# Kernel tuning notes

Hardware: AMD Instinct MI355X
Metric: run time of the kernel (lower is better)

The kernel has to match this reference:

```python
import jax, jax.numpy as jnp
import numpy as np

B, T, C, H = 2, 512, 1024, 16
D = C // H          # head dim 64
CS = 64             # chunk_size
NS_STEPS = 5
OMEGA_W = 8
KCONV = 4

# Polar Express per-iteration quintic coefficients (Amsel et al. 2025)
_PE_COEFFS = [
    (8.28721201814563, -23.595886519098837, 17.300387312530933),
    (4.107059111542203, -2.9478499167379106, 0.5448431082926601),
    (3.9486908534822946, -2.908902115962949, 0.5518191394370137),
    (3.3184196573706015, -2.488488024314874, 0.51004894012372),
    (2.300652019954817, -1.6689039845747493, 0.4188073119525673),
    (1.891301407787398, -1.2679958271945868, 0.37680408948524835),
    (1.8750014808534479, -1.2500016453999487, 0.3750001645474248),
    (1.875, -1.25, 0.375),
]

def _polar_express(X):
    # X: (..., D, D). Normalize to spectral-norm <= 1 via Frobenius bound, then iterate.
    nrm = jnp.sqrt(jnp.sum(X * X, axis=(-2, -1), keepdims=True)) + 1e-7
    Xn = X / (nrm * 1.01)
    for a, b, c in _PE_COEFFS[:NS_STEPS]:
        A = Xn @ jnp.swapaxes(Xn, -1, -2)
        Xn = a * Xn + (b * A + c * (A @ A)) @ Xn
    return Xn

def _polar_express_ste(X):
    # straight-through: forward = PE(X), backward = identity
    return X + jax.lax.stop_gradient(_polar_express(X) - X)

def _rms_norm(x):
    return x * jax.lax.rsqrt(jnp.mean(x * x, axis=-1, keepdims=True) + 1e-6)

def _poly_features(x):
    # phi(x) = sum_{i=1..p} x^i / i!  with poly_degree=2
    return x + 0.5 * x * x

def _short_conv(x, w, b):
    # causal depthwise conv; x:(B,T,C), w:(C,1,K), b:(C,)
    xc = jnp.transpose(x, (0, 2, 1))
    xc = jnp.pad(xc, ((0, 0), (0, 0), (KCONV - 1, 0)))
    y = jax.lax.conv_general_dilated(
        xc, w, window_strides=(1,), padding="VALID",
        dimension_numbers=("NCW", "OIW", "NCW"), feature_group_count=x.shape[-1])
    y = y + b[:, None]
    return jnp.transpose(y, (0, 2, 1))

def _linear_scan(h_init, gates, inputs):
    # h_t = g_t * h_{t-1} + in_t ; gates (B,cs,H), inputs (B,cs,H,D,D)
    g = gates[..., None, None]
    first = g[:, :1] * h_init[:, None] + inputs[:, :1]
    mod_in = jnp.concatenate([first, inputs[:, 1:]], axis=1)
    mod_g = jnp.concatenate([jnp.zeros_like(g[:, :1]), g[:, 1:]], axis=1)
    def comb(a, b):
        ga, xa = a; gb, xb = b
        return (ga * gb, gb * xa + xb)
    _, h_all = jax.lax.associative_scan(comb, (mod_g, mod_in), axis=1)
    return h_all, h_all[:, -1]

def _omega_aggregate(u, gamma):
    # sliding-window sum of gamma_i * u_i over last OMEGA_W positions, via cumsum
    cs = u.shape[1]
    cum = jnp.cumsum(gamma * u, axis=1)
    if OMEGA_W >= cs:
        return cum
    shifted = jnp.concatenate([jnp.zeros_like(cum[:, :OMEGA_W]), cum[:, :-OMEGA_W]], axis=1)
    return cum - shifted


def setup_inputs() -> dict:
    key = jax.random.key(0)
    ks = jax.random.split(key, 16)
    s = 0.02
    return {
        "x":   jax.random.normal(ks[0], (B, T, C), jnp.float32),
        "Wq":  jax.random.normal(ks[1], (C, C), jnp.float32) * s,
        "Wk":  jax.random.normal(ks[2], (C, C), jnp.float32) * s,
        "Wv":  jax.random.normal(ks[3], (C, C), jnp.float32) * s,
        "Wo":  jax.random.normal(ks[4], (C, C), jnp.float32) * s,
        "cqw": jax.random.normal(ks[5], (C, 1, KCONV), jnp.float32) * s,
        "cqb": jnp.zeros((C,), jnp.float32),
        "ckw": jax.random.normal(ks[6], (C, 1, KCONV), jnp.float32) * s,
        "ckb": jnp.zeros((C,), jnp.float32),
        "cvw": jax.random.normal(ks[7], (C, 1, KCONV), jnp.float32) * s,
        "cvb": jnp.zeros((C,), jnp.float32),
        "Wa":  jax.random.normal(ks[8], (H, C), jnp.float32) * s,
        "We":  jax.random.normal(ks[9], (H, C), jnp.float32) * s,
        "Wt":  jax.random.normal(ks[10], (H, C), jnp.float32) * s,
        "Wg":  jax.random.normal(ks[11], (H, C), jnp.float32) * s,
    }


def reference(x, Wq, Wk, Wv, Wo, cqw, cqb, ckw, ckb, cvw, cvb, Wa, We, Wt, Wg):
    Bsz, Tlen, Cdim = x.shape
    q = _short_conv(x @ Wq.T, cqw, cqb).reshape(Bsz, Tlen, H, D)
    k = _short_conv(x @ Wk.T, ckw, ckb).reshape(Bsz, Tlen, H, D)
    v = _short_conv(x @ Wv.T, cvw, cvb).reshape(Bsz, Tlen, H, D)
    q = _poly_features(_rms_norm(q))
    k = _poly_features(_rms_norm(k))
    alpha = jax.nn.sigmoid(x @ Wa.T)   # (B,T,H) memory retention gate
    eta   = jax.nn.sigmoid(x @ We.T)   # learning rate gate
    theta = jax.nn.sigmoid(x @ Wt.T)   # momentum gate
    gamma = jax.nn.sigmoid(x @ Wg.T)   # omega context gate

    nC = Tlen // CS
    def chunked(a):  # (B,T,...) -> (nC,B,CS,...)
        return jnp.moveaxis(a.reshape(Bsz, nC, CS, *a.shape[2:]), 1, 0)
    qc, kc, vc = chunked(q), chunked(k), chunked(v)
    ac, ec, tc, gc = chunked(alpha), chunked(eta), chunked(theta), chunked(gamma)

    M0 = jnp.zeros((Bsz, H, D, D), x.dtype)
    S0 = jnp.zeros((Bsz, H, D, D), x.dtype)

    def step(carry, inp):
        M, S = carry
        q_c, k_c, v_c, a_c, e_c, t_c, g_c = inp
        pred = jnp.einsum("bhvk,bchk->bchv", M, k_c)
        err = pred - v_c
        u = 2.0 * jnp.einsum("bchv,bchk->bchvk", err, k_c)     # per-token gradient
        u = _omega_aggregate(u, g_c[..., None, None])           # omega window
        mom_in = -(e_c[..., None, None] * u)
        chunk_S, S = _linear_scan(S, t_c, mom_in)               # momentum scan
        chunk_S_orth = _polar_express_ste(chunk_S)              # orthogonalize
        M_all, M = _linear_scan(M, a_c, chunk_S_orth)           # memory scan
        y_c = jnp.einsum("bchvk,bchk->bchv", M_all, q_c)        # read memory
        return (M, S), y_c

    _, ys = jax.lax.scan(step, (M0, S0), (qc, kc, vc, ac, ec, tc, gc))
    y = jnp.moveaxis(ys, 0, 1).reshape(Bsz, Tlen, H, D)
    y = _rms_norm(y).reshape(Bsz, Tlen, Cdim)
    return y @ Wo.T
```

## Files before the change

### kernel.cpp

```cpp
#include <hip/hip_runtime.h>

constexpr int Bsz = 2, Tsz = 512, Csz = 1024, Hsz = 16, Dsz = 64, CSz = 64;
constexpr int NCHUNK = 8, OW = 8;

typedef __attribute__((ext_vector_type(8))) _Float16 half8;
typedef __attribute__((ext_vector_type(4))) _Float16 half4;
typedef __attribute__((ext_vector_type(2))) _Float16 half2v;
typedef __attribute__((ext_vector_type(2))) __fp16 fp16x2;
typedef __attribute__((ext_vector_type(16))) float f32x16;

constexpr float INV_S = 1.0f / 2048.0f;

union H4u { half4 v; half2v p[2]; };

__device__ __forceinline__ void split_f16(float v, _Float16& hi, _Float16& lo) {
  _Float16 h = (_Float16)v;
  float r = v - (float)h;
  hi = h;
  lo = (_Float16)(r * 2048.0f);
}

__device__ __forceinline__ void split2(float a, float b, half2v& h, half2v& l) {
  fp16x2 hh = __builtin_amdgcn_cvt_pkrtz(a, b);
  half2v hv = __builtin_bit_cast(half2v, hh);
  float ra = (a - (float)hv[0]) * 2048.0f;
  float rb = (b - (float)hv[1]) * 2048.0f;
  h = hv;
  l = __builtin_bit_cast(half2v, __builtin_amdgcn_cvt_pkrtz(ra, rb));
}

#define MFMA3(accH, accL1, accL2, ah, al, bh, bl)                             \
  accH = __builtin_amdgcn_mfma_f32_32x32x16_f16(ah, bh, accH, 0, 0, 0);       \
  accL1 = __builtin_amdgcn_mfma_f32_32x32x16_f16(ah, bl, accL1, 0, 0, 0);     \
  accL2 = __builtin_amdgcn_mfma_f32_32x32x16_f16(al, bh, accL2, 0, 0, 0);

__device__ __forceinline__ void xcd_decode(int bid, int& bh, int& idx) {
  bh = (((bid >> 3) & 3) << 3) + (bid & 7);
  idx = bid >> 5;
}

__global__ __launch_bounds__(256) void split_all_kernel(
    const float* __restrict__ x, const float* __restrict__ Wq,
    const float* __restrict__ Wk, const float* __restrict__ Wv,
    const float* __restrict__ Wo, const float* __restrict__ Wa,
    const float* __restrict__ We, const float* __restrict__ Wt,
    const float* __restrict__ Wg,
    _Float16* __restrict__ xh, _Float16* __restrict__ xl,
    _Float16* __restrict__ Wqh, _Float16* __restrict__ Wql,
    _Float16* __restrict__ Wkh, _Float16* __restrict__ Wkl,
    _Float16* __restrict__ Wvh, _Float16* __restrict__ Wvl,
    _Float16* __restrict__ Woh, _Float16* __restrict__ Wol,
    _Float16* __restrict__ gWh, _Float16* __restrict__ gWl) {
  const int y = blockIdx.y;
  const int tid = threadIdx.x;
  if (y < 5) {
    const float* src = (y == 0 ? x : y == 1 ? Wq : y == 2 ? Wk : y == 3 ? Wv : Wo);
    _Float16* dh = (y == 0 ? xh : y == 1 ? Wqh : y == 2 ? Wkh : y == 3 ? Wvh : Woh);
    _Float16* dl = (y == 0 ? xl : y == 1 ? Wql : y == 2 ? Wkl : y == 3 ? Wvl : Wol);
    size_t i = ((size_t)blockIdx.x * 256 + tid) * 4;
    float4 v = *(const float4*)(src + i);
    H4u h, l;
    split2(v.x, v.y, h.p[0], l.p[0]);
    split2(v.z, v.w, h.p[1], l.p[1]);
    *(half4*)(dh + i) = h.v;
    *(half4*)(dl + i) = l.v;
  } else {
    if (blockIdx.x >= 64) return;
    size_t i = ((size_t)blockIdx.x * 256 + tid) * 4;
    int gsel = (int)(i >> 14);
    int off = (int)(i & 16383);
    const float* src = (gsel == 0 ? Wa : gsel == 1 ? We : gsel == 2 ? Wt : Wg);
    float4 v = *(const float4*)(src + off);
    H4u h, l;
    split2(v.x, v.y, h.p[0], l.p[0]);
    split2(v.z, v.w, h.p[1], l.p[1]);
    *(half4*)(gWh + i) = h.v;
    *(half4*)(gWl + i) = l.v;
  }
}

__device__ __forceinline__ void gemm64_core(const _Float16* __restrict__ Agh,
                                            const _Float16* __restrict__ Agl,
                                            const _Float16* __restrict__ Bgh,
                                            const _Float16* __restrict__ Bgl,
                                            int m0, int n0, int tid, char* LB,
                                            f32x16& accH, f32x16& accL1, f32x16& accL2) {
  const int lane = tid & 63, wv = tid >> 6;
  const int mb = (wv >> 1) << 5, nb = (wv & 1) << 5;
  const int lr = tid >> 2;
  const int lch = (tid & 3) << 4;
  const int cb = lch << 1;
  const int wb0 = (lr << 7) + (cb ^ ((lr & 7) << 4));
  const int wb1 = (lr << 7) + ((cb + 16) ^ ((lr & 7) << 4));
  const _Float16* pah = Agh + (size_t)(m0 + lr) * Csz + lch;
  const _Float16* pal = Agl + (size_t)(m0 + lr) * Csz + lch;
  const _Float16* pbh = Bgh + (size_t)(n0 + lr) * Csz + lch;
  const _Float16* pbl = Bgl + (size_t)(n0 + lr) * Csz + lch;
  int ra_m[4], ra_n[4];
#pragma unroll
  for (int ks = 0; ks < 4; ++ks) {
    int rm = mb + (lane & 31), rn = nb + (lane & 31);
    int cB = (ks << 5) + ((lane >> 5) << 4);
    ra_m[ks] = (rm << 7) + (cB ^ ((rm & 7) << 4));
    ra_n[ks] = (rn << 7) + (cB ^ ((rn & 7) << 4));
  }
#pragma unroll
  for (int r = 0; r < 16; ++r) { accH[r] = 0.f; accL1[r] = 0.f; accL2[r] = 0.f; }
  for (int k0 = 0; k0 < Csz; k0 += 64) {
    half8 vah0 = *(const half8*)(pah + k0), vah1 = *(const half8*)(pah + k0 + 8);
    half8 val0 = *(const half8*)(pal + k0), val1 = *(const half8*)(pal + k0 + 8);
    half8 vbh0 = *(const half8*)(pbh + k0), vbh1 = *(const half8*)(pbh + k0 + 8);
    half8 vbl0 = *(const half8*)(pbl + k0), vbl1 = *(const half8*)(pbl + k0 + 8);
    __syncthreads();
    *(half8*)(LB + wb0) = vah0;          *(half8*)(LB + wb1) = vah1;
    *(half8*)(LB + 8192 + wb0) = val0;   *(half8*)(LB + 8192 + wb1) = val1;
    *(half8*)(LB + 16384 + wb0) = vbh0;  *(half8*)(LB + 16384 + wb1) = vbh1;
    *(half8*)(LB + 24576 + wb0) = vbl0;  *(half8*)(LB + 24576 + wb1) = vbl1;
    __syncthreads();
    __builtin_amdgcn_s_setprio(1);
#pragma unroll
    for (int ks = 0; ks < 4; ++ks) {
      half8 ah = *(const half8*)(LB + ra_m[ks]);
      half8 al = *(const half8*)(LB + 8192 + ra_m[ks]);
      half8 bh = *(const half8*)(LB + 16384 + ra_n[ks]);
      half8 bl = *(const half8*)(LB + 24576 + ra_n[ks]);
      MFMA3(accH, accL1, accL2, ah, al, bh, bl);
    }
    __builtin_amdgcn_s_setprio(0);
  }
}

__global__ __launch_bounds__(256) void qkvg_mfma(
    const _Float16* __restrict__ xh, const _Float16* __restrict__ xl,
    const _Float16* __restrict__ Wqh, const _Float16* __restrict__ Wql,
    const _Float16* __restrict__ Wkh, const _Float16* __restrict__ Wkl,
    const _Float16* __restrict__ Wvh, const _Float16* __restrict__ Wvl,
    const _Float16* __restrict__ gWh, const _Float16* __restrict__ gWl,
    float* __restrict__ qlin, float* __restrict__ klin, float* __restrict__ vlin,
    float* __restrict__ ga, float* __restrict__ ge,
    float* __restrict__ gt, float* __restrict__ gg) {
  __shared__ __attribute__((aligned(16))) char LB[32768];
  const int tid = threadIdx.x;
  const int by = blockIdx.y;
  const int m0 = blockIdx.x << 6;
  const _Float16 *Bh, *Bl;
  int n0;
  if (by < 48) {
    const int mat = by >> 4;
    n0 = (by & 15) << 6;
    Bh = (mat == 0 ? Wqh : mat == 1 ? Wkh : Wvh);
    Bl = (mat == 0 ? Wql : mat == 1 ? Wkl : Wvl);
  } else {
    n0 = 0;
    Bh = gWh;
    Bl = gWl;
  }
  f32x16 accH, accL1, accL2;
  gemm64_core(xh, xl, Bh, Bl, m0, n0, tid, LB, accH, accL1, accL2);
  const int lane = tid & 63, wv = tid >> 6;
  const int mb = (wv >> 1) << 5, nb = (wv & 1) << 5;
  const int crow = (lane >> 5) << 2, ccol = lane & 31;
  if (by < 48) {
    const int mat = by >> 4;
    float* O = (mat == 0 ? qlin : mat == 1 ? klin : vlin);
#pragma unroll
    for (int r = 0; r < 16; ++r) {
      int row = mb + crow + (r & 3) + ((r >> 2) << 3);
      O[(size_t)(m0 + row) * Csz + n0 + nb + ccol] = accH[r] + (accL1[r] + accL2[r]) * INV_S;
    }
  } else {
    const int col = nb + ccol;
    const int gsel = col >> 4, h = col & 15;
    float* outp = (gsel == 0 ? ga : gsel == 1 ? ge : gsel == 2 ? gt : gg);
#pragma unroll
    for (int r = 0; r < 16; ++r) {
      int row = mb + crow + (r & 3) + ((r >> 2) << 3);
      float v = accH[r] + (accL1[r] + accL2[r]) * INV_S;
      outp[(size_t)(m0 + row) * Hsz + h] = 1.f / (1.f + expf(-v));
    }
  }
}

__global__ __launch_bounds__(256) void out_mfma(
    const _Float16* __restrict__ yh, const _Float16* __restrict__ yl,
    const _Float16* __restrict__ Woh, const _Float16* __restrict__ Wol,
    float* __restrict__ out) {
  __shared__ __attribute__((aligned(16))) char LB[32768];
  const int tid = threadIdx.x;
  const int m0 = blockIdx.x << 6, n0 = blockIdx.y << 6;
  f32x16 accH, accL1, accL2;
  gemm64_core(yh, yl, Woh, Wol, m0, n0, tid, LB, accH, accL1, accL2);
  const int lane = tid & 63, wv = tid >> 6;
  const int mb = (wv >> 1) << 5, nb = (wv & 1) << 5;
  const int crow = (lane >> 5) << 2, ccol = lane & 31;
#pragma unroll
  for (int r = 0; r < 16; ++r) {
    int row = mb + crow + (r & 3) + ((r >> 2) << 3);
    out[(size_t)(m0 + row) * Csz + n0 + nb + ccol] = accH[r] + (accL1[r] + accL2[r]) * INV_S;
  }
}

__global__ __launch_bounds__(256) void conv3_kernel(const float* __restrict__ qlin,
                                                    const float* __restrict__ klin,
                                                    const float* __restrict__ vlin,
                                                    const float* __restrict__ cqw,
                                                    const float* __restrict__ ckw,
                                                    const float* __restrict__ cvw,
                                                    const float* __restrict__ cqb,
                                                    const float* __restrict__ ckb,
                                                    const float* __restrict__ cvb,
                                                    float* __restrict__ qp,
                                                    float* __restrict__ kp,
                                                    float* __restrict__ vp) {
  const int sel = blockIdx.y;
  const float* lin = (sel == 0 ? qlin : sel == 1 ? klin : vlin);
  const float* w = (sel == 0 ? cqw : sel == 1 ? ckw : cvw);
  const float* bias = (sel == 0 ? cqb : sel == 1 ? ckb : cvb);
  float* out = (sel == 0 ? qp : sel == 1 ? kp : vp);
  const int do_norm = (sel < 2);
  const int bt = blockIdx.x;
  const int b = bt >> 9, t = bt & 511;
  const int tid = threadIdx.x;
  const int c0 = tid << 2;
  float4 bv = *(const float4*)&bias[c0];
  float v0 = bv.x, v1 = bv.y, v2 = bv.z, v3 = bv.w;
  float4 w0 = *(const float4*)&w[(c0 + 0) * 4];
  float4 w1 = *(const float4*)&w[(c0 + 1) * 4];
  float4 w2 = *(const float4*)&w[(c0 + 2) * 4];
  float4 w3 = *(const float4*)&w[(c0 + 3) * 4];
  const float* base = lin + (size_t)b * Tsz * Csz + c0;
#pragma unroll
  for (int j = 0; j < 4; ++j) {
    int tt = t - 3 + j;
    if (tt < 0) continue;
    float4 xv = *(const float4*)(base + (size_t)tt * Csz);
    v0 += xv.x * (&w0.x)[j];
    v1 += xv.y * (&w1.x)[j];
    v2 += xv.z * (&w2.x)[j];
    v3 += xv.w * (&w3.x)[j];
  }
  if (do_norm) {
    float ss = v0 * v0 + v1 * v1 + v2 * v2 + v3 * v3;
    ss += __shfl_xor(ss, 1, 16);
    ss += __shfl_xor(ss, 2, 16);
    ss += __shfl_xor(ss, 4, 16);
    ss += __shfl_xor(ss, 8, 16);
    float scl = rsqrtf(ss * (1.f / 64.f) + 1e-6f);
    v0 *= scl; v1 *= scl; v2 *= scl; v3 *= scl;
    v0 += 0.5f * v0 * v0; v1 += 0.5f * v1 * v1; v2 += 0.5f * v2 * v2; v3 += 0.5f * v3 * v3;
  }
  float4 o = {v0, v1, v2, v3};
  *(float4*)(out + (size_t)bt * Csz + c0) = o;
}

__global__ __launch_bounds__(256) void rms_split_kernel(const float* __restrict__ in,
                                                        _Float16* __restrict__ yh,
                                                        _Float16* __restrict__ yl) {
  const int bt = blockIdx.x;
  const int tid = threadIdx.x;
  const int c0 = tid << 2;
  float4 xv = *(const float4*)(in + (size_t)bt * Csz + c0);
  float ss = xv.x * xv.x + xv.y * xv.y + xv.z * xv.z + xv.w * xv.w;
  ss += __shfl_xor(ss, 1, 16);
  ss += __shfl_xor(ss, 2, 16);
  ss += __shfl_xor(ss, 4, 16);
  ss += __shfl_xor(ss, 8, 16);
  float scl = rsqrtf(ss * (1.f / 64.f) + 1e-6f);
  H4u h, l;
  split2(xv.x * scl, xv.y * scl, h.p[0], l.p[0]);
  split2(xv.z * scl, xv.w * scl, h.p[1], l.p[1]);
  *(half4*)(yh + (size_t)bt * Csz + c0) = h.v;
  *(half4*)(yl + (size_t)bt * Csz + c0) = l.v;
}

__global__ __launch_bounds__(256) void mom_scan_kernel(const float* __restrict__ Mst,
                                                       const float* __restrict__ kp,
                                                       const float* __restrict__ vp,
                                                       const float* __restrict__ geta,
                                                       const float* __restrict__ gtheta,
                                                       const float* __restrict__ ggamma,
                                                       float* __restrict__ Sst,
                                                       float* __restrict__ chunkS, int ci) {
  __shared__ float Ml[4 * Dsz];
  __shared__ float errl[256];
  __shared__ float kkl[CSz * Dsz];
  __shared__ float gl[CSz], el[CSz], tl[CSz];
  int bh, eb;
  xcd_decode(blockIdx.x, bh, eb);
  const int b = bh >> 4, h = bh & 15;
  const int tid = threadIdx.x;
  const int e = eb * 256 + tid;
  float S = Sst[(size_t)bh * 4096 + e];
  const int tt0 = tid >> 2, vl0 = tid & 3;
  float vv = vp[(((size_t)b * Tsz + ci * CSz + tt0) * Hsz + h) * Dsz + eb * 4 + vl0];
  Ml[tid & 255] = Mst[(size_t)bh * 4096 + eb * 4 * 64 + tid];
#pragma unroll
  for (int i = 0; i < 16; ++i) {
    int idx = i * 256 + tid;
    int t = idx >> 6, k = idx & 63;
    kkl[idx] = kp[(((size_t)b * Tsz + ci * CSz + t) * Hsz + h) * Dsz + k];
  }
  if (tid < CSz) {
    size_t gi = ((size_t)b * Tsz + ci * CSz + tid) * Hsz + h;
    gl[tid] = ggamma[gi];
    el[tid] = geta[gi];
    tl[tid] = gtheta[gi];
  }
  __syncthreads();
  {
    float acc = 0.f;
#pragma unroll
    for (int i = 0; i < 16; ++i) {
      float4 m4 = *(const float4*)&Ml[vl0 * 64 + i * 4];
      float4 k4 = *(const float4*)&kkl[tt0 * 64 + i * 4];
      acc += m4.x * k4.x + m4.y * k4.y + m4.z * k4.z + m4.w * k4.w;
    }
    errl[tt0 * 4 + vl0] = acc - vv;
  }
  __syncthreads();
  const int vloc = tid >> 6;
  const int k = tid & 63;
  float ring[OW];
  float wsum = 0.f;
  float* outp = chunkS + (size_t)bh * CSz * 4096 + e;
#pragma unroll
  for (int t = 0; t < CSz; ++t) {
    float u = 2.f * errl[t * 4 + vloc] * kkl[t * 64 + k];
    float val = gl[t] * u;
    wsum += val;
    if (t >= OW) wsum -= ring[t & (OW - 1)];
    ring[t & (OW - 1)] = val;
    S = tl[t] * S - el[t] * wsum;
    outp[(size_t)t * 4096] = S;
  }
  Sst[(size_t)bh * 4096 + e] = S;
}

__global__ __launch_bounds__(256) void fused_scan_kernel(float* __restrict__ chunkS,
                                                         const float* __restrict__ qp,
                                                         const float* __restrict__ kp,
                                                         const float* __restrict__ vp,
                                                         const float* __restrict__ galpha,
                                                         const float* __restrict__ geta,
                                                         const float* __restrict__ gtheta,
                                                         const float* __restrict__ ggamma,
                                                         float* __restrict__ Mst,
                                                         float* __restrict__ Sst,
                                                         float* __restrict__ ybuf,
                                                         int ci, int do_next) {
  __shared__ float buf[CSz * Dsz];
  __shared__ float al[CSz];
  __shared__ float Ml[4 * Dsz];
  __shared__ float errl[256];
  __shared__ float gl[CSz], el[CSz], tl[CSz];
  int bh, eb;
  xcd_decode(blockIdx.x, bh, eb);
  const int b = bh >> 4, h = bh & 15;
  const int tid = threadIdx.x;
  const int w = tid >> 6, lane = tid & 63;
  const int v = eb * 4 + w, k = lane;
  float m = Mst[(size_t)bh * 4096 + v * 64 + k];
  for (int i = tid; i < CSz * Dsz; i += 256) {
    int t = i >> 6, kk = i & 63;
    buf[i] = qp[(((size_t)b * Tsz + ci * CSz + t) * Hsz + h) * Dsz + kk];
  }
  if (tid < CSz) al[tid] = galpha[((size_t)b * Tsz + ci * CSz + tid) * Hsz + h];
  __syncthreads();
  const float* Xp = chunkS + (size_t)bh * CSz * 4096 + v * 64 + k;
  float* yb = ybuf + (((size_t)b * Tsz + ci * CSz) * Hsz + h) * Dsz + v;
  float x0 = Xp[0], x1 = Xp[4096], x2 = Xp[8192], x3 = Xp[12288];
  for (int t0 = 0; t0 < CSz; t0 += 4) {
    float n0, n1, n2, n3;
    if (t0 + 4 < CSz) {
      const float* Xn = Xp + (size_t)(t0 + 4) * 4096;
      n0 = Xn[0]; n1 = Xn[4096]; n2 = Xn[8192]; n3 = Xn[12288];
    } else {
      n0 = n1 = n2 = n3 = 0.f;
    }
    float m0 = al[t0] * m + x0;
    float m1 = al[t0 + 1] * m0 + x1;
    float m2 = al[t0 + 2] * m1 + x2;
    float m3 = al[t0 + 3] * m2 + x3;
    m = m3;
    float p0 = m0 * buf[(t0 + 0) * 64 + k];
    float p1 = m1 * buf[(t0 + 1) * 64 + k];
    float p2 = m2 * buf[(t0 + 2) * 64 + k];
    float p3 = m3 * buf[(t0 + 3) * 64 + k];
#pragma unroll
    for (int off = 32; off; off >>= 1) {
      p0 += __shfl_xor(p0, off, 64);
      p1 += __shfl_xor(p1, off, 64);
      p2 += __shfl_xor(p2, off, 64);
      p3 += __shfl_xor(p3, off, 64);
    }
    if (lane < 4) {
      float pj = (lane == 0 ? p0 : lane == 1 ? p1 : lane == 2 ? p2 : p3);
      yb[(size_t)(t0 + lane) * Hsz * Dsz] = pj;
    }
    x0 = n0; x1 = n1; x2 = n2; x3 = n3;
  }
  Mst[(size_t)bh * 4096 + v * 64 + k] = m;
  if (!do_next) return;
  const int cj = ci + 1;
  const int e = eb * 256 + tid;
  float S = Sst[(size_t)bh * 4096 + e];
  const int tt0 = tid >> 2, vl0 = tid & 3;
  float vv = vp[(((size_t)b * Tsz + cj * CSz + tt0) * Hsz + h) * Dsz + eb * 4 + vl0];
  Ml[w * 64 + k] = m;
  __syncthreads();
#pragma unroll
  for (int i = 0; i < 16; ++i) {
    int idx = i * 256 + tid;
    int t = idx >> 6, kk = idx & 63;
    buf[idx] = kp[(((size_t)b * Tsz + cj * CSz + t) * Hsz + h) * Dsz + kk];
  }
  if (tid < CSz) {
    size_t gi = ((size_t)b * Tsz + cj * CSz + tid) * Hsz + h;
    gl[tid] = ggamma[gi];
    el[tid] = geta[gi];
    tl[tid] = gtheta[gi];
  }
  __syncthreads();
  {
    float acc = 0.f;
#pragma unroll
    for (int i = 0; i < 16; ++i) {
      float4 m4 = *(const float4*)&Ml[vl0 * 64 + i * 4];
      float4 k4 = *(const float4*)&buf[tt0 * 64 + i * 4];
      acc += m4.x * k4.x + m4.y * k4.y + m4.z * k4.z + m4.w * k4.w;
    }
    errl[tt0 * 4 + vl0] = acc - vv;
  }
  __syncthreads();
  const int vloc = tid >> 6;
  float ring[OW];
  float wsum = 0.f;
  float* outp = chunkS + (size_t)bh * CSz * 4096 + e;
#pragma unroll
  for (int t = 0; t < CSz; ++t) {
    float u = 2.f * errl[t * 4 + vloc] * buf[t * 64 + k];
    float val = gl[t] * u;
    wsum += val;
    if (t >= OW) wsum -= ring[t & (OW - 1)];
    ring[t & (OW - 1)] = val;
    S = tl[t] * S - el[t] * wsum;
    outp[(size_t)t * 4096] = S;
  }
  Sst[(size_t)bh * 4096 + e] = S;
}

__global__ __launch_bounds__(256, 3) void pe_mfma_kernel(float* __restrict__ chunkS) {
  __shared__ __attribute__((aligned(16))) _Float16 PL[6 * 4096];
  __shared__ float red[4];
  const int tid = threadIdx.x;
  const int lane = tid & 63;
  const int wv = tid >> 6;
  int bh, tmat;
  xcd_decode(blockIdx.x, bh, tmat);
  float* G = chunkS + ((size_t)bh * CSz + tmat) * 4096;
  constexpr int PLO = 8192;
  constexpr int PT = 16384;
  char* const LB = (char*)PL;

  const int mb = (wv >> 1) << 5;
  const int nb = (wv & 1) << 5;
  const int crow = ((lane >> 5) << 2);
  const int ccol = lane & 31;

  int ra_m[4], ra_n[4];
#pragma unroll
  for (int ks = 0; ks < 4; ++ks) {
    int rm = mb + (lane & 31), rn = nb + (lane & 31);
    int cB = (ks << 5) + ((lane >> 5) << 4);
    ra_m[ks] = (rm << 7) + (cB ^ ((rm & 7) << 4));
    ra_n[ks] = (rn << 7) + (cB ^ ((rn & 7) << 4));
  }
  int sa[4];
  {
    const int base = (nb + ccol) << 7;
    const int sw = ((nb + ccol) & 7) << 4;
    const int c2 = crow << 1;
#pragma unroll
    for (int g = 0; g < 4; ++g) sa[g] = base + ((((mb + 8 * g) << 1) ^ sw) + c2);
  }
  int rowa[4];
#pragma unroll
  for (int j = 0; j < 4; ++j) {
    int rr = mb + crow + j;
    rowa[j] = (rr << 7) + (((nb + ccol) << 1) ^ ((rr & 7) << 4));
  }

#define LDF(PB, RA, ks) (*(const half8*)(LB + (PB) + (RA)[ks]))

  auto STS = [&](int PB, const half2v* h2, const half2v* l2) {
#pragma unroll
    for (int g = 0; g < 4; ++g) {
      H4u hu, lu;
      hu.p[0] = h2[2 * g]; hu.p[1] = h2[2 * g + 1];
      lu.p[0] = l2[2 * g]; lu.p[1] = l2[2 * g + 1];
      *(half4*)(LB + PB + sa[g]) = hu.v;
      *(half4*)(LB + PB + PLO + sa[g]) = lu.v;
    }
  };
  auto STR = [&](int PB, const half2v* h2, const half2v* l2) {
#pragma unroll
    for (int r = 0; r < 16; ++r) {
      int off = rowa[r & 3] + ((r >> 2) << 10);
      *(_Float16*)(LB + PB + off) = h2[r >> 1][r & 1];
      *(_Float16*)(LB + PB + PLO + off) = l2[r >> 1][r & 1];
    }
  };

  float Xval[16];
  float ss = 0.f;
#pragma unroll
  for (int r = 0; r < 16; ++r) {
    int rr = mb + crow + (r & 3) + ((r >> 2) << 3);
    float xv = G[rr * 64 + nb + ccol];
    Xval[r] = xv;
    ss += xv * xv;
  }
#pragma unroll
  for (int off = 32; off; off >>= 1) ss += __shfl_xor(ss, off, 64);
  if (lane == 0) red[wv] = ss;
  __syncthreads();
  float tot = red[0] + red[1] + red[2] + red[3];
  float scale = 1.f / ((sqrtf(tot) + 1e-7f) * 1.01f);

  {
    half2v hs2[8], ls2[8];
#pragma unroll
    for (int i = 0; i < 8; ++i) {
      Xval[2 * i] *= scale;
      Xval[2 * i + 1] *= scale;
      split2(Xval[2 * i], Xval[2 * i + 1], hs2[i], ls2[i]);
    }
    STR(0, hs2, ls2);
    STS(PT, hs2, ls2);
  }

  auto iter = [&](float ca, float cb, float cc, int PXB, int PAB, bool last) {
    __syncthreads();
    half8 pth[4], ptl[4];
    {
      f32x16 accH, accL1, accL2;
#pragma unroll
      for (int r = 0; r < 16; ++r) { accH[r] = 0.f; accL1[r] = 0.f; accL2[r] = 0.f; }
      __builtin_amdgcn_s_setprio(1);
#pragma unroll
      for (int ks = 0; ks < 4; ++ks) {
        half8 ah = LDF(PXB, ra_m, ks), al = LDF(PXB + PLO, ra_m, ks);
        half8 bh, bl;
        if (mb != nb) { bh = LDF(PXB, ra_n, ks); bl = LDF(PXB + PLO, ra_n, ks); }
        else { bh = ah; bl = al; }
        MFMA3(accH, accL1, accL2, ah, al, bh, bl);
      }
      __builtin_amdgcn_s_setprio(0);
#pragma unroll
      for (int ks = 0; ks < 4; ++ks) {
        pth[ks] = LDF(PT, ra_n, ks);
        ptl[ks] = LDF(PT + PLO, ra_n, ks);
      }
      half2v hs2[8], ls2[8];
#pragma unroll
      for (int i = 0; i < 8; ++i) {
        float a0 = accH[2 * i] + (accL1[2 * i] + accL2[2 * i]) * INV_S;
        float a1 = accH[2 * i + 1] + (accL1[2 * i + 1] + accL2[2 * i + 1]) * INV_S;
        split2(a0, a1, hs2[i], ls2[i]);
      }
      STS(PAB, hs2, ls2);
    }
    __syncthreads();
    half8 fah[4], fal[4];
    f32x16 acWH, acWL1, acWL2;
#pragma unroll
    for (int r = 0; r < 16; ++r) { acWH[r] = 0.f; acWL1[r] = 0.f; acWL2[r] = 0.f; }
    __builtin_amdgcn_s_setprio(1);
#pragma unroll
    for (int ks = 0; ks < 4; ++ks) {
      fah[ks] = LDF(PAB, ra_m, ks);
      fal[ks] = LDF(PAB + PLO, ra_m, ks);
      MFMA3(acWH, acWL1, acWL2, fah[ks], fal[ks], pth[ks], ptl[ks]);
    }
    __builtin_amdgcn_s_setprio(0);
    float Wval[16];
    {
      half2v hs2[8], ls2[8];
#pragma unroll
      for (int i = 0; i < 8; ++i) {
        Wval[2 * i] = acWH[2 * i] + (acWL1[2 * i] + acWL2[2 * i]) * INV_S;
        Wval[2 * i + 1] = acWH[2 * i + 1] + (acWL1[2 * i + 1] + acWL2[2 * i + 1]) * INV_S;
        split2(Wval[2 * i], Wval[2 * i + 1], hs2[i], ls2[i]);
      }
      STS(PXB, hs2, ls2);
    }
    __syncthreads();
    f32x16 acUH, acUL1, acUL2;
#pragma unroll
    for (int r = 0; r < 16; ++r) { acUH[r] = 0.f; acUL1[r] = 0.f; acUL2[r] = 0.f; }
    __builtin_amdgcn_s_setprio(1);
#pragma unroll
    for (int ks = 0; ks < 4; ++ks) {
      half8 bh = LDF(PXB, ra_n, ks), bl = LDF(PXB + PLO, ra_n, ks);
      MFMA3(acUH, acUL1, acUL2, fah[ks], fal[ks], bh, bl);
    }
    __builtin_amdgcn_s_setprio(0);
    if (!last) {
      half2v hs2[8], ls2[8];
#pragma unroll
      for (int i = 0; i < 8; ++i) {
        float u0 = acUH[2 * i] + (acUL1[2 * i] + acUL2[2 * i]) * INV_S;
        float u1 = acUH[2 * i + 1] + (acUL1[2 * i + 1] + acUL2[2 * i + 1]) * INV_S;
        float x0 = ca * Xval[2 * i] + cb * Wval[2 * i] + cc * u0;
        float x1 = ca * Xval[2 * i + 1] + cb * Wval[2 * i + 1] + cc * u1;
        Xval[2 * i] = x0;
        Xval[2 * i + 1] = x1;
        split2(x0, x1, hs2[i], ls2[i]);
      }
      STR(PAB, hs2, ls2);
      STS(PT, hs2, ls2);
    } else {
#pragma unroll
      for (int r = 0; r < 16; ++r) {
        int rr = mb + crow + (r & 3) + ((r >> 2) << 3);
        float u = acUH[r] + (acUL1[r] + acUL2[r]) * INV_S;
        G[rr * 64 + nb + ccol] = ca * Xval[r] + cb * Wval[r] + cc * u;
      }
    }
  };

  iter(8.28721201814563f, -23.595886519098837f, 17.300387312530933f, 0, 32768, false);
  iter(4.107059111542203f, -2.9478499167379106f, 0.5448431082926601f, 32768, 0, false);
  iter(3.9486908534822946f, -2.908902115962949f, 0.5518191394370137f, 0, 32768, false);
  iter(3.3184196573706015f, -2.488488024314874f, 0.51004894012372f, 32768, 0, false);
  iter(2.300652019954817f, -1.6689039845747493f, 0.4188073119525673f, 0, 32768, true);
}

extern "C" void kernel_launch(void* const* d_in, const int* in_sizes, int n_in,
                              void* d_out, int out_size, void* d_ws, size_t ws_size,
                              hipStream_t stream) {
  (void)in_sizes; (void)n_in; (void)out_size; (void)ws_size;
  const float* x   = (const float*)d_in[0];
  const float* Wq  = (const float*)d_in[1];
  const float* Wk  = (const float*)d_in[2];
  const float* Wv  = (const float*)d_in[3];
  const float* Wo  = (const float*)d_in[4];
  const float* cqw = (const float*)d_in[5];
  const float* cqb = (const float*)d_in[6];
  const float* ckw = (const float*)d_in[7];
  const float* ckb = (const float*)d_in[8];
  const float* cvw = (const float*)d_in[9];
  const float* cvb = (const float*)d_in[10];
  const float* Wa  = (const float*)d_in[11];
  const float* We  = (const float*)d_in[12];
  const float* Wt  = (const float*)d_in[13];
  const float* Wg  = (const float*)d_in[14];
  float* out = (float*)d_out;

  float* p = (float*)d_ws;
  const size_t NBTC = (size_t)Bsz * Tsz * Csz;
  const size_t NBTH = (size_t)Bsz * Tsz * Hsz;
  const size_t NMAT = (size_t)Bsz * Hsz * Dsz * Dsz;
  const size_t NWW = (size_t)Csz * Csz;
  float* qlin = p; p += NBTC;
  float* klin = p; p += NBTC;
  float* vlin = p; p += NBTC;
  float* qp   = p; p += NBTC;
  float* kp   = p; p += NBTC;
  float* vp   = p; p += NBTC;
  float* ga   = p; p += NBTH;
  float* ge   = p; p += NBTH;
  float* gt   = p; p += NBTH;
  float* gg   = p; p += NBTH;
  float* Mst  = p; p += NMAT;
  float* Sst  = p; p += NMAT;
  float* chS  = p; p += (size_t)Bsz * Hsz * CSz * Dsz * Dsz;
  float* ybuf = p; p += NBTC;
  _Float16* hp = (_Float16*)p;
  _Float16* xh  = hp; hp += NBTC;
  _Float16* xl  = hp; hp += NBTC;
  _Float16* Wqh = hp; hp += NWW;
  _Float16* Wql = hp; hp += NWW;
  _Float16* Wkh = hp; hp += NWW;
  _Float16* Wkl = hp; hp += NWW;
  _Float16* Wvh = hp; hp += NWW;
  _Float16* Wvl = hp; hp += NWW;
  _Float16* Woh = hp; hp += NWW;
  _Float16* Wol = hp; hp += NWW;
  _Float16* gWh = hp; hp += (size_t)64 * Csz;
  _Float16* gWl = hp; hp += (size_t)64 * Csz;
  _Float16* yh  = hp; hp += NBTC;
  _Float16* yl  = hp; hp += NBTC;

  hipMemsetAsync(Mst, 0, NMAT * sizeof(float), stream);
  hipMemsetAsync(Sst, 0, NMAT * sizeof(float), stream);

  split_all_kernel<<<dim3(1024, 6), 256, 0, stream>>>(
      x, Wq, Wk, Wv, Wo, Wa, We, Wt, Wg,
      xh, xl, Wqh, Wql, Wkh, Wkl, Wvh, Wvl, Woh, Wol, gWh, gWl);
  qkvg_mfma<<<dim3(16, 49), 256, 0, stream>>>(
      xh, xl, Wqh, Wql, Wkh, Wkl, Wvh, Wvl, gWh, gWl,
      qlin, klin, vlin, ga, ge, gt, gg);
  conv3_kernel<<<dim3(Bsz * Tsz, 3), 256, 0, stream>>>(qlin, klin, vlin, cqw, ckw, cvw,
                                                       cqb, ckb, cvb, qp, kp, vp);

  mom_scan_kernel<<<Bsz * Hsz * 16, 256, 0, stream>>>(Mst, kp, vp, ge, gt, gg, Sst, chS, 0);
  for (int ci = 0; ci < NCHUNK; ++ci) {
    pe_mfma_kernel<<<Bsz * Hsz * CSz, 256, 0, stream>>>(chS);
    fused_scan_kernel<<<Bsz * Hsz * 16, 256, 0, stream>>>(chS, qp, kp, vp, ga, ge, gt, gg,
                                                          Mst, Sst, ybuf, ci,
                                                          ci < NCHUNK - 1 ? 1 : 0);
  }

  rms_split_kernel<<<Bsz * Tsz, 256, 0, stream>>>(ybuf, yh, yl);
  out_mfma<<<dim3(16, 16), 256, 0, stream>>>(yh, yl, Woh, Wol, out);
}
```

Baseline: 869.4 us.

## Prefetch GEMM tiles, preload memory-scan inputs, fold PE combine into MFMA accumulator

The split-fp16 GEMM loop now issues the next K-tile's global loads after the LDS stores, so they overlap with the MFMAs instead of stalling before the barrier. The memory-scan kernel loads all 64 chunk-state values per thread into registers up front rather than prefetching four at a time. The Polar Express iteration seeds the final MFMA accumulator with (a/c)X + (b/c)W, which removes a separate combine pass afterwards. The costs are higher register pressure (a 64-float array) and a small numerical change from dividing by c and reassociating the sums.

Result: faster. 823.5 us (-5.3%).

```diff
diff --git a/kernel.cpp b/kernel.cpp
--- a/kernel.cpp
+++ b/kernel.cpp
@@ -106,17 +106,23 @@
   }
 #pragma unroll
   for (int r = 0; r < 16; ++r) { accH[r] = 0.f; accL1[r] = 0.f; accL2[r] = 0.f; }
+  half8 vah0 = *(const half8*)(pah), vah1 = *(const half8*)(pah + 8);
+  half8 val0 = *(const half8*)(pal), val1 = *(const half8*)(pal + 8);
+  half8 vbh0 = *(const half8*)(pbh), vbh1 = *(const half8*)(pbh + 8);
+  half8 vbl0 = *(const half8*)(pbl), vbl1 = *(const half8*)(pbl + 8);
   for (int k0 = 0; k0 < Csz; k0 += 64) {
-    half8 vah0 = *(const half8*)(pah + k0), vah1 = *(const half8*)(pah + k0 + 8);
-    half8 val0 = *(const half8*)(pal + k0), val1 = *(const half8*)(pal + k0 + 8);
-    half8 vbh0 = *(const half8*)(pbh + k0), vbh1 = *(const half8*)(pbh + k0 + 8);
-    half8 vbl0 = *(const half8*)(pbl + k0), vbl1 = *(const half8*)(pbl + k0 + 8);
     __syncthreads();
     *(half8*)(LB + wb0) = vah0;          *(half8*)(LB + wb1) = vah1;
     *(half8*)(LB + 8192 + wb0) = val0;   *(half8*)(LB + 8192 + wb1) = val1;
     *(half8*)(LB + 16384 + wb0) = vbh0;  *(half8*)(LB + 16384 + wb1) = vbh1;
     *(half8*)(LB + 24576 + wb0) = vbl0;  *(half8*)(LB + 24576 + wb1) = vbl1;
     __syncthreads();
+    if (k0 + 64 < Csz) {
+      vah0 = *(const half8*)(pah + k0 + 64); vah1 = *(const half8*)(pah + k0 + 72);
+      val0 = *(const half8*)(pal + k0 + 64); val1 = *(const half8*)(pal + k0 + 72);
+      vbh0 = *(const half8*)(pbh + k0 + 64); vbh1 = *(const half8*)(pbh + k0 + 72);
+      vbl0 = *(const half8*)(pbl + k0 + 64); vbl1 = *(const half8*)(pbl + k0 + 72);
+    }
     __builtin_amdgcn_s_setprio(1);
 #pragma unroll
     for (int ks = 0; ks < 4; ++ks) {
@@ -368,19 +374,15 @@
   __syncthreads();
   const float* Xp = chunkS + (size_t)bh * CSz * 4096 + v * 64 + k;
   float* yb = ybuf + (((size_t)b * Tsz + ci * CSz) * Hsz + h) * Dsz + v;
-  float x0 = Xp[0], x1 = Xp[4096], x2 = Xp[8192], x3 = Xp[12288];
+  float xv[CSz];
+#pragma unroll
+  for (int t = 0; t < CSz; ++t) xv[t] = Xp[(size_t)t * 4096];
+#pragma unroll
   for (int t0 = 0; t0 < CSz; t0 += 4) {
-    float n0, n1, n2, n3;
-    if (t0 + 4 < CSz) {
-      const float* Xn = Xp + (size_t)(t0 + 4) * 4096;
-      n0 = Xn[0]; n1 = Xn[4096]; n2 = Xn[8192]; n3 = Xn[12288];
-    } else {
-      n0 = n1 = n2 = n3 = 0.f;
-    }
-    float m0 = al[t0] * m + x0;
-    float m1 = al[t0 + 1] * m0 + x1;
-    float m2 = al[t0 + 2] * m1 + x2;
-    float m3 = al[t0 + 3] * m2 + x3;
+    float m0 = al[t0] * m + xv[t0];
+    float m1 = al[t0 + 1] * m0 + xv[t0 + 1];
+    float m2 = al[t0 + 2] * m1 + xv[t0 + 2];
+    float m3 = al[t0 + 3] * m2 + xv[t0 + 3];
     m = m3;
     float p0 = m0 * buf[(t0 + 0) * 64 + k];
     float p1 = m1 * buf[(t0 + 1) * 64 + k];
@@ -397,7 +399,6 @@
       float pj = (lane == 0 ? p0 : lane == 1 ? p1 : lane == 2 ? p2 : p3);
       yb[(size_t)(t0 + lane) * Hsz * Dsz] = pj;
     }
-    x0 = n0; x1 = n1; x2 = n2; x3 = n3;
   }
   Mst[(size_t)bh * 4096 + v * 64 + k] = m;
   if (!do_next) return;
@@ -540,6 +541,7 @@
   }
 
   auto iter = [&](float ca, float cb, float cc, int PXB, int PAB, bool last) {
+    const float rca = ca / cc, rcb = cb / cc, ccS = cc * INV_S;
     __syncthreads();
     half8 pth[4], ptl[4];
     {
@@ -597,7 +599,10 @@
     __syncthreads();
     f32x16 acUH, acUL1, acUL2;
 #pragma unroll
-    for (int r = 0; r < 16; ++r) { acUH[r] = 0.f; acUL1[r] = 0.f; acUL2[r] = 0.f; }
+    for (int r = 0; r < 16; ++r) {
+      acUH[r] = rca * Xval[r] + rcb * Wval[r];
+      acUL1[r] = 0.f; acUL2[r] = 0.f;
+    }
     __builtin_amdgcn_s_setprio(1);
 #pragma unroll
     for (int ks = 0; ks < 4; ++ks) {
@@ -609,10 +614,8 @@
       half2v hs2[8], ls2[8];
 #pragma unroll
       for (int i = 0; i < 8; ++i) {
-        float u0 = acUH[2 * i] + (acUL1[2 * i] + acUL2[2 * i]) * INV_S;
-        float u1 = acUH[2 * i + 1] + (acUL1[2 * i + 1] + acUL2[2 * i + 1]) * INV_S;
-        float x0 = ca * Xval[2 * i] + cb * Wval[2 * i] + cc * u0;
-        float x1 = ca * Xval[2 * i + 1] + cb * Wval[2 * i + 1] + cc * u1;
+        float x0 = cc * acUH[2 * i] + ccS * (acUL1[2 * i] + acUL2[2 * i]);
+        float x1 = cc * acUH[2 * i + 1] + ccS * (acUL1[2 * i + 1] + acUL2[2 * i + 1]);
         Xval[2 * i] = x0;
         Xval[2 * i + 1] = x1;
         split2(x0, x1, hs2[i], ls2[i]);
@@ -623,8 +626,7 @@
 #pragma unroll
       for (int r = 0; r < 16; ++r) {
         int rr = mb + crow + (r & 3) + ((r >> 2) << 3);
-        float u = acUH[r] + (acUL1[r] + acUL2[r]) * INV_S;
-        G[rr * 64 + nb + ccol] = ca * Xval[r] + cb * Wval[r] + cc * u;
+        G[rr * 64 + nb + ccol] = cc * acUH[r] + ccS * (acUL1[r] + acUL2[r]);
       }
     }
   };
```
